# Optimization experiments

Hardware: AMD Instinct MI355X
Metric: run time of the kernel (lower is better)

The kernel has to match this reference:

```python
import jax, jax.numpy as jnp
import numpy as np

N_NODES = 16384
HID_IN = 1024   # hid_size (GCN in/out dim)
HID_MID = 1500  # hidden_size
N_EDGES = 131072


def setup_inputs() -> dict:
    key = jax.random.key(0)
    k1, k2, k3, k4, k5, k6 = jax.random.split(key, 6)
    x = jax.random.normal(k1, (N_NODES, HID_IN), dtype=jnp.float32)
    edge_index = jax.random.randint(k2, (2, N_EDGES), 0, N_NODES, dtype=jnp.int64)
    # GCNConv weights (glorot-ish scale) and biases
    W1 = jax.random.normal(k3, (HID_IN, HID_MID), dtype=jnp.float32) / np.sqrt(HID_IN)
    b1 = jnp.zeros((HID_MID,), dtype=jnp.float32)
    W2 = jax.random.normal(k4, (HID_MID, HID_IN), dtype=jnp.float32) / np.sqrt(HID_MID)
    b2 = jnp.zeros((HID_IN,), dtype=jnp.float32)
    return {"x": x, "edge_index": edge_index, "W1": W1, "b1": b1, "W2": W2, "b2": b2}


def _gcn_conv(x, W, b, src, dst, inv_sqrt_deg, n_nodes):
    # PyG GCNConv: out[i] = sum_{(j->i)} d_j^{-1/2} d_i^{-1/2} (x W)[j] + b
    h = x @ W                                   # [N, out]
    norm = inv_sqrt_deg[src] * inv_sqrt_deg[dst]  # [E]
    msg = h[src] * norm[:, None]                 # gather + scale [E, out]
    out = jax.ops.segment_sum(msg, dst, num_segments=n_nodes)
    return out + b


def reference(x, edge_index, W1, b1, W2, b2):
    n = x.shape[0]
    # add self-loops (GCNConv default)
    loops = jnp.arange(n, dtype=edge_index.dtype)
    src = jnp.concatenate([edge_index[0], loops])
    dst = jnp.concatenate([edge_index[1], loops])
    deg = jax.ops.segment_sum(jnp.ones_like(dst, dtype=x.dtype), dst, num_segments=n)
    inv_sqrt_deg = jnp.where(deg > 0, jax.lax.rsqrt(jnp.maximum(deg, 1.0)), 0.0)
    h = _gcn_conv(x, W1, b1, src, dst, inv_sqrt_deg, n)
    h = jax.nn.relu(h)  # dropout skipped (eval mode)
    out = _gcn_conv(h, W2, b2, src, dst, inv_sqrt_deg, n)
    return out
```

## Files before the change

kernel.cpp:

```cpp
#include <hip/hip_runtime.h>
#include <cstdint>
#include <cstddef>

#define NN 16384
#define DIN 1024
#define DMID 1500
#define DMIDP 1536
#define NE 131072

typedef __bf16 bf16;
typedef __bf16 bf16x4 __attribute__((ext_vector_type(4)));
typedef __bf16 bf16x8 __attribute__((ext_vector_type(8)));
typedef float f32x4 __attribute__((ext_vector_type(4)));

#define GLOBAL_AS __attribute__((address_space(1)))
#define LDS_AS __attribute__((address_space(3)))

__device__ __forceinline__ void gload_lds16(const bf16* g, bf16* l) {
    __builtin_amdgcn_global_load_lds((GLOBAL_AS const unsigned int*)(g),
                                     (LDS_AS unsigned int*)(l), 16, 0, 0);
}

#define SBAR() asm volatile("s_barrier" ::: "memory")
#define WAITV_(N) asm volatile("s_waitcnt vmcnt(" #N ")" ::: "memory")
#define WAITV(N) WAITV_(N)
#define WAITL0() asm volatile("s_waitcnt lgkmcnt(0)" ::: "memory")

__global__ void k_zero_cnt(int* cnt) {
    cnt[blockIdx.x * 256 + threadIdx.x] = 0;
}

__global__ void k_count(const int* __restrict__ dst, int* cnt) {
    int e = blockIdx.x * 256 + threadIdx.x;
    atomicAdd(&cnt[dst[e]], 1);
}

__global__ __launch_bounds__(1024) void k_scan(const int* __restrict__ cnt,
                                               int* __restrict__ rowptr,
                                               int* __restrict__ cursor,
                                               float* __restrict__ isd) {
    __shared__ int sums[1024];
    int t = threadIdx.x;
    int base = t * 16;
    int v[16], p[16];
    int s = 0;
#pragma unroll
    for (int k = 0; k < 16; ++k) {
        v[k] = cnt[base + k];
        p[k] = (v[k] + 7) & ~7;
        s += p[k];
    }
    sums[t] = s;
    __syncthreads();
    for (int off = 1; off < 1024; off <<= 1) {
        int y = (t >= off) ? sums[t - off] : 0;
        __syncthreads();
        sums[t] += y;
        __syncthreads();
    }
    int run = sums[t] - s;
#pragma unroll
    for (int k = 0; k < 16; ++k) {
        rowptr[base + k] = run;
        cursor[base + k] = run;
        isd[base + k] = rsqrtf((float)(v[k] + 1));
        run += p[k];
    }
    if (t == 1023) rowptr[NN] = run;
}

__global__ void k_fill(const int* __restrict__ src, const int* __restrict__ dst,
                       int* cursor, const float* __restrict__ isd,
                       int* __restrict__ csr_src, float* __restrict__ csr_w) {
    int e = blockIdx.x * 256 + threadIdx.x;
    int s = src[e], d = dst[e];
    int pos = atomicAdd(&cursor[d], 1);
    csr_src[pos] = s;
    csr_w[pos] = isd[s] * isd[d];
}

__global__ void k_pad(const int* __restrict__ cnt, const int* __restrict__ rowptr,
                      int* __restrict__ csr_src, float* __restrict__ csr_w) {
    int i = blockIdx.x * 256 + threadIdx.x;
    int c = cnt[i];
    int p = (c + 7) & ~7;
    int base = rowptr[i];
    for (int q = c; q < p; ++q) {
        csr_src[base + q] = i;
        csr_w[base + q] = 0.0f;
    }
}

__global__ void k_cvt_x(const float4* __restrict__ x, bf16x4* __restrict__ xb) {
    int i = blockIdx.x * 256 + threadIdx.x;
    float4 v = x[i];
    bf16x4 o;
    o[0] = (bf16)v.x; o[1] = (bf16)v.y; o[2] = (bf16)v.z; o[3] = (bf16)v.w;
    xb[i] = o;
}


__global__ __launch_bounds__(256) void k_cvt_w1(const float* __restrict__ W1,
                                                bf16* __restrict__ W1b) {
    __shared__ float t[32][33];
    int n0 = blockIdx.x * 32;
    int k0 = blockIdx.y * 32;
    int tx = threadIdx.x & 31, ty = threadIdx.x >> 5;
#pragma unroll
    for (int p = 0; p < 4; ++p) {
        int n = n0 + tx;
        t[p * 8 + ty][tx] = (n < DMID)
            ? W1[(size_t)(k0 + p * 8 + ty) * DMID + n] : 0.0f;
    }
    __syncthreads();
#pragma unroll
    for (int p = 0; p < 4; ++p) {
        int n = n0 + p * 8 + ty;
        W1b[(size_t)n * DIN + k0 + tx] = (bf16)t[tx][p * 8 + ty];
    }
}

__global__ __launch_bounds__(256) void k_cvt_w2(const float* __restrict__ W2,
                                                bf16* __restrict__ W2b) {
    __shared__ float t[32][33];
    int n0 = blockIdx.x * 32;
    int k0 = blockIdx.y * 32;
    int tx = threadIdx.x & 31, ty = threadIdx.x >> 5;
#pragma unroll
    for (int p = 0; p < 4; ++p) {
        int k = k0 + p * 8 + ty;
        t[p * 8 + ty][tx] = (k < DMID)
            ? W2[(size_t)k * DIN + n0 + tx] : 0.0f;
    }
    __syncthreads();
#pragma unroll
    for (int p = 0; p < 4; ++p) {
        int n = n0 + p * 8 + ty;
        W2b[(size_t)n * DMIDP + k0 + tx] = (bf16)t[tx][p * 8 + ty];
    }
}

template <int K, int N, bool RELU_BIAS>
__global__ __launch_bounds__(256, 2) void gemm128(const bf16* __restrict__ A,
                                                  const bf16* __restrict__ Bt,
                                                  bf16* __restrict__ C,
                                                  const float* __restrict__ bias) {
    constexpr int NT = K / 64;
    __shared__ __align__(16) bf16 ldsA[2][128 * 64];
    __shared__ __align__(16) bf16 ldsB[2][128 * 64];
    const int tid = threadIdx.x;
    const int w = tid >> 6;
    const int lane = tid & 63;
    const int bm = blockIdx.x, bn = blockIdx.y;
    const int fr = lane & 15, fq = lane >> 4;
    const int wm = w & 1;
    const int wn = w >> 1;
    const int sx = fr & 7;

    const int lrow = lane >> 3;
    const int lslot = (lane & 7) ^ lrow;
    const bf16* gA = A + (size_t)(bm * 128 + w * 32 + lrow) * K + lslot * 8;
    const bf16* gB = Bt + (size_t)(bn * 128 + w * 32 + lrow) * K + lslot * 8;

    f32x4 acc[4][4];
#pragma unroll
    for (int i = 0; i < 4; ++i)
#pragma unroll
        for (int j = 0; j < 4; ++j) acc[i][j] = {0.f, 0.f, 0.f, 0.f};

#define STAGE(T, BUF)                                                          \
    do {                                                                       \
        _Pragma("unroll") for (int r = 0; r < 4; ++r)                          \
            gload_lds16(gA + (size_t)(T) * 64 + (size_t)(r * 8) * K,           \
                        &ldsA[BUF][0] + w * 2048 + r * 512);                   \
        _Pragma("unroll") for (int r = 0; r < 4; ++r)                          \
            gload_lds16(gB + (size_t)(T) * 64 + (size_t)(r * 8) * K,           \
                        &ldsB[BUF][0] + w * 2048 + r * 512);                   \
    } while (0)

    STAGE(0, 0);
    STAGE(1, 1);
    WAITV(8);
    SBAR();

    for (int t = 0; t < NT; ++t) {
        const int c = t & 1;
#pragma unroll
        for (int ks = 0; ks < 2; ++ks) {
            bf16x8 bq[4], af[4];
#pragma unroll
            for (int nt = 0; nt < 4; ++nt) {
                int row = wn * 64 + nt * 16 + fr;
                int sl = ((ks << 2) | fq) ^ sx;
                bq[nt] = *(const bf16x8*)((const char*)&ldsB[c][0] +
                                          row * 128 + sl * 16);
            }
#pragma unroll
            for (int mt = 0; mt < 4; ++mt) {
                int row = wm * 64 + mt * 16 + fr;
                int sl = ((ks << 2) | fq) ^ sx;
                af[mt] = *(const bf16x8*)((const char*)&ldsA[c][0] +
                                          row * 128 + sl * 16);
            }
            __builtin_amdgcn_s_setprio(1);
#pragma unroll
            for (int mt = 0; mt < 4; ++mt)
#pragma unroll
                for (int nt = 0; nt < 4; ++nt)
                    acc[mt][nt] = __builtin_amdgcn_mfma_f32_16x16x32_bf16(
                        af[mt], bq[nt], acc[mt][nt], 0, 0, 0);
            __builtin_amdgcn_s_setprio(0);
        }
        if (t + 1 < NT) {
            WAITL0();
            WAITV(0);
            SBAR();
            if (t + 2 < NT) STAGE(t + 2, c);
        }
    }
#undef STAGE

    float bv[4];
    if (RELU_BIAS) {
#pragma unroll
        for (int nt = 0; nt < 4; ++nt) {
            int col = bn * 128 + wn * 64 + nt * 16 + fr;
            bv[nt] = (col < DMID) ? bias[col] : 0.0f;
        }
    }
#pragma unroll
    for (int mq = 0; mq < 4; ++mq) {
        int row0 = bm * 128 + wm * 64 + mq * 16 + fq * 4;
#pragma unroll
        for (int nt = 0; nt < 4; ++nt) {
            int col = bn * 128 + wn * 64 + nt * 16 + fr;
#pragma unroll
            for (int r = 0; r < 4; ++r) {
                float v = acc[mq][nt][r];
                if (RELU_BIAS) v = fmaxf(v + bv[nt], 0.0f);
                C[(size_t)(row0 + r) * N + col] = (bf16)v;
            }
        }
    }
}


__global__ __launch_bounds__(128) void k_aggX(const bf16* __restrict__ X,
                                              const int* __restrict__ rowptr,
                                              const int* __restrict__ csr_src,
                                              const float* __restrict__ csr_w,
                                              const float* __restrict__ isd,
                                              bf16* __restrict__ XA) {
    int i = blockIdx.x;
    int t = threadIdx.x;
    int c0 = t * 8;
    int beg = rowptr[i], end = rowptr[i + 1];
    float wi = isd[i];
    float w0 = wi * wi;
    float a[8];
    bf16x8 h = *(const bf16x8*)&X[(size_t)i * DIN + c0];
#pragma unroll
    for (int k = 0; k < 8; ++k) a[k] = w0 * (float)h[k];
    for (int e = beg; e < end; e += 8) {
        int j[8];
        float w[8];
        bf16x8 hv[8];
#pragma unroll
        for (int q = 0; q < 8; ++q) { j[q] = csr_src[e + q]; w[q] = csr_w[e + q]; }
#pragma unroll
        for (int q = 0; q < 8; ++q)
            hv[q] = *(const bf16x8*)&X[(size_t)j[q] * DIN + c0];
#pragma unroll
        for (int q = 0; q < 8; ++q)
#pragma unroll
            for (int k = 0; k < 8; ++k) a[k] += w[q] * (float)hv[q][k];
    }
    bf16x8 o;
#pragma unroll
    for (int k = 0; k < 8; ++k) o[k] = (bf16)a[k];
    *(bf16x8*)&XA[(size_t)i * DIN + c0] = o;
}

__global__ __launch_bounds__(128) void k_agg2(const bf16* __restrict__ H,
                                              const int* __restrict__ rowptr,
                                              const int* __restrict__ csr_src,
                                              const float* __restrict__ csr_w,
                                              const float* __restrict__ isd,
                                              const float* __restrict__ b2,
                                              float* __restrict__ out) {
    int i = blockIdx.x;
    int t = threadIdx.x;
    int c0 = t * 8;
    int beg = rowptr[i], end = rowptr[i + 1];
    float wi = isd[i];
    float w0 = wi * wi;
    float a[8];
    bf16x8 h = *(const bf16x8*)&H[(size_t)i * DIN + c0];
#pragma unroll
    for (int k = 0; k < 8; ++k) a[k] = w0 * (float)h[k];
    for (int e = beg; e < end; e += 8) {
        int j[8];
        float w[8];
        bf16x8 hv[8];
#pragma unroll
        for (int q = 0; q < 8; ++q) { j[q] = csr_src[e + q]; w[q] = csr_w[e + q]; }
#pragma unroll
        for (int q = 0; q < 8; ++q)
            hv[q] = *(const bf16x8*)&H[(size_t)j[q] * DIN + c0];
#pragma unroll
        for (int q = 0; q < 8; ++q)
#pragma unroll
            for (int k = 0; k < 8; ++k) a[k] += w[q] * (float)hv[q][k];
    }
    float4 o0, o1;
    o0.x = a[0] + b2[c0 + 0]; o0.y = a[1] + b2[c0 + 1];
    o0.z = a[2] + b2[c0 + 2]; o0.w = a[3] + b2[c0 + 3];
    o1.x = a[4] + b2[c0 + 4]; o1.y = a[5] + b2[c0 + 5];
    o1.z = a[6] + b2[c0 + 6]; o1.w = a[7] + b2[c0 + 7];
    *(float4*)&out[(size_t)i * DIN + c0] = o0;
    *(float4*)&out[(size_t)i * DIN + c0 + 4] = o1;
}

extern "C" void kernel_launch(void* const* d_in, const int* in_sizes, int n_in,
                              void* d_out, int out_size, void* d_ws, size_t ws_size,
                              hipStream_t stream) {
    const float* x = (const float*)d_in[0];
    const int* ei = (const int*)d_in[1];
    const float* W1 = (const float*)d_in[2];
    const float* b1 = (const float*)d_in[3];
    const float* W2 = (const float*)d_in[4];
    const float* b2 = (const float*)d_in[5];
    float* out = (float*)d_out;
    const int* src = ei;
    const int* dst = ei + NE;

    char* ws = (char*)d_ws;
    int* cnt      = (int*)(ws + 0);
    int* cursor   = (int*)(ws + 65536);
    float* isd    = (float*)(ws + 131072);
    int* rowptr   = (int*)(ws + 196608);
    int* csr_src  = (int*)(ws + 327680);
    float* csr_w  = (float*)(ws + 2424832);
    bf16* Xb      = (bf16*)(ws + 4521984);
    bf16* XA      = (bf16*)(ws + 38076416);
    bf16* W1b     = (bf16*)(ws + 71630848);
    bf16* W2b     = (bf16*)(ws + 74776576);
    bf16* Y1b     = (bf16*)(ws + 77922304);
    bf16* H2b     = XA;

    k_zero_cnt<<<NN / 256, 256, 0, stream>>>(cnt);
    k_count<<<NE / 256, 256, 0, stream>>>(dst, cnt);
    k_scan<<<1, 1024, 0, stream>>>(cnt, rowptr, cursor, isd);
    k_fill<<<NE / 256, 256, 0, stream>>>(src, dst, cursor, isd, csr_src, csr_w);
    k_pad<<<NN / 256, 256, 0, stream>>>(cnt, rowptr, csr_src, csr_w);

    k_cvt_x<<<NN * DIN / 4 / 256, 256, 0, stream>>>((const float4*)x, (bf16x4*)Xb);
    {
        dim3 gw1(DMIDP / 32, DIN / 32);
        k_cvt_w1<<<gw1, 256, 0, stream>>>(W1, W1b);
        dim3 gw2(DIN / 32, DMIDP / 32);
        k_cvt_w2<<<gw2, 256, 0, stream>>>(W2, W2b);
    }

    k_aggX<<<NN, 128, 0, stream>>>(Xb, rowptr, csr_src, csr_w, isd, XA);
    dim3 g1(NN / 128, DMIDP / 128);
    gemm128<DIN, DMIDP, true><<<g1, 256, 0, stream>>>(XA, W1b, Y1b, b1);

    dim3 g2(NN / 128, DIN / 128);
    gemm128<DMIDP, DIN, false><<<g2, 256, 0, stream>>>(Y1b, W2b, H2b, nullptr);
    k_agg2<<<NN, 128, 0, stream>>>(H2b, rowptr, csr_src, csr_w, isd, b2, out);
}
```

Baseline: 370.8 us.

## Replace double-buffered GEMM pipeline with single-buffer sync loop and higher occupancy

Removes the two-stage LDS double buffering and manual vmcnt/barrier scheduling from the bf16 MFMA GEMM. Each K-tile is now loaded into a single LDS buffer, followed by __syncthreads before and after compute. LDS per block is halved and launch bounds raised to 4 blocks per CU, so more resident blocks are meant to hide latency instead of explicit prefetching. The cost is that loads no longer overlap compute within a block, and 4 blocks per CU caps registers per thread more tightly, which could cause spills for the 64-float accumulator tile.

Result: no change. 366.1 us (-1.3%).

```diff
diff --git a/kernel.cpp b/kernel.cpp
--- a/kernel.cpp
+++ b/kernel.cpp
@@ -20,11 +20,6 @@
     __builtin_amdgcn_global_load_lds((GLOBAL_AS const unsigned int*)(g),
                                      (LDS_AS unsigned int*)(l), 16, 0, 0);
 }
-
-#define SBAR() asm volatile("s_barrier" ::: "memory")
-#define WAITV_(N) asm volatile("s_waitcnt vmcnt(" #N ")" ::: "memory")
-#define WAITV(N) WAITV_(N)
-#define WAITL0() asm volatile("s_waitcnt lgkmcnt(0)" ::: "memory")
 
 __global__ void k_zero_cnt(int* cnt) {
     cnt[blockIdx.x * 256 + threadIdx.x] = 0;
@@ -141,13 +136,13 @@
 }
 
 template <int K, int N, bool RELU_BIAS>
-__global__ __launch_bounds__(256, 2) void gemm128(const bf16* __restrict__ A,
+__global__ __launch_bounds__(256, 4) void gemm128(const bf16* __restrict__ A,
                                                   const bf16* __restrict__ Bt,
                                                   bf16* __restrict__ C,
                                                   const float* __restrict__ bias) {
     constexpr int NT = K / 64;
-    __shared__ __align__(16) bf16 ldsA[2][128 * 64];
-    __shared__ __align__(16) bf16 ldsB[2][128 * 64];
+    __shared__ __align__(16) bf16 ldsA[128 * 64];
+    __shared__ __align__(16) bf16 ldsB[128 * 64];
     const int tid = threadIdx.x;
     const int w = tid >> 6;
     const int lane = tid & 63;
@@ -168,23 +163,16 @@
 #pragma unroll
         for (int j = 0; j < 4; ++j) acc[i][j] = {0.f, 0.f, 0.f, 0.f};
 
-#define STAGE(T, BUF)                                                          \
-    do {                                                                       \
-        _Pragma("unroll") for (int r = 0; r < 4; ++r)                          \
-            gload_lds16(gA + (size_t)(T) * 64 + (size_t)(r * 8) * K,           \
-                        &ldsA[BUF][0] + w * 2048 + r * 512);                   \
-        _Pragma("unroll") for (int r = 0; r < 4; ++r)                          \
-            gload_lds16(gB + (size_t)(T) * 64 + (size_t)(r * 8) * K,           \
-                        &ldsB[BUF][0] + w * 2048 + r * 512);                   \
-    } while (0)
-
-    STAGE(0, 0);
-    STAGE(1, 1);
-    WAITV(8);
-    SBAR();
-
     for (int t = 0; t < NT; ++t) {
-        const int c = t & 1;
+#pragma unroll
+        for (int r = 0; r < 4; ++r)
+            gload_lds16(gA + (size_t)t * 64 + (size_t)(r * 8) * K,
+                        &ldsA[0] + w * 2048 + r * 512);
+#pragma unroll
+        for (int r = 0; r < 4; ++r)
+            gload_lds16(gB + (size_t)t * 64 + (size_t)(r * 8) * K,
+                        &ldsB[0] + w * 2048 + r * 512);
+        __syncthreads();
 #pragma unroll
         for (int ks = 0; ks < 2; ++ks) {
             bf16x8 bq[4], af[4];
@@ -192,14 +180,14 @@
             for (int nt = 0; nt < 4; ++nt) {
                 int row = wn * 64 + nt * 16 + fr;
                 int sl = ((ks << 2) | fq) ^ sx;
-                bq[nt] = *(const bf16x8*)((const char*)&ldsB[c][0] +
+                bq[nt] = *(const bf16x8*)((const char*)&ldsB[0] +
                                           row * 128 + sl * 16);
             }
 #pragma unroll
             for (int mt = 0; mt < 4; ++mt) {
                 int row = wm * 64 + mt * 16 + fr;
                 int sl = ((ks << 2) | fq) ^ sx;
-                af[mt] = *(const bf16x8*)((const char*)&ldsA[c][0] +
+                af[mt] = *(const bf16x8*)((const char*)&ldsA[0] +
                                           row * 128 + sl * 16);
             }
             __builtin_amdgcn_s_setprio(1);
@@ -211,14 +199,8 @@
                         af[mt], bq[nt], acc[mt][nt], 0, 0, 0);
             __builtin_amdgcn_s_setprio(0);
         }
-        if (t + 1 < NT) {
-            WAITL0();
-            WAITV(0);
-            SBAR();
-            if (t + 2 < NT) STAGE(t + 2, c);
-        }
-    }
-#undef STAGE
+        __syncthreads();
+    }
 
     float bv[4];
     if (RELU_BIAS) {
```
